# Kernel optimization log

Hardware: AMD Instinct MI355X
Metric: run time of the kernel (lower is better)

## Reference

```python
import jax, jax.numpy as jnp
import numpy as np

TOP_K = 4
EPS = 1e-12  # torch F.normalize eps

def _l2_normalize(x):
    n = jnp.linalg.norm(x, axis=-1, keepdims=True)
    return x / jnp.maximum(n, EPS)

def setup_inputs() -> dict:
    key = jax.random.key(0)
    k1, k2, k3 = jax.random.split(key, 3)
    queries = jax.random.normal(k1, (8192, 768), dtype=jnp.float32)
    # nn.init.uniform_(-1, 1) for both params
    keys = jax.random.uniform(k2, (64, 768), dtype=jnp.float32, minval=-1.0, maxval=1.0)
    prompts = jax.random.uniform(k3, (64, 8, 768), dtype=jnp.float32, minval=-1.0, maxval=1.0)
    return {"queries": queries, "keys": keys, "prompts": prompts}

def reference(queries, keys, prompts):
    N = queries.shape[0]
    pool_size, prompt_dim, embed_dim = prompts.shape
    qn = _l2_normalize(queries)              # [N, D]
    kn = _l2_normalize(keys)                 # [P, D]
    sim = qn @ kn.T                          # [N, P] cosine similarity
    _, idx = jax.lax.top_k(sim, TOP_K)       # [N, K] per-query top-k key ids
    # histogram vote over the pool (equivalent to torch.unique(..., return_counts) + pad)
    counts = jnp.zeros((pool_size,), jnp.int32).at[idx.reshape(-1)].add(1)
    _, top_idx = jax.lax.top_k(counts, TOP_K)  # [K] most-voted prompt ids
    # gather prompts, broadcast to every query: [N, K*prompt_dim, embed_dim]
    sel = prompts[top_idx].reshape(1, TOP_K * prompt_dim, embed_dim)
    selected_prompts = jnp.broadcast_to(sel, (N, TOP_K * prompt_dim, embed_dim))
    selected_keys = kn[top_idx]              # [K, D], same for all queries
    loss = jnp.sum(selected_keys[None, :, :] * qn[:, None, :]) / N
    return selected_prompts, loss
```

## Files before the change

kernel.cpp:

```cpp
#include <hip/hip_runtime.h>
#include <math.h>

#define NQ 8192
#define D 768
#define DF4 (D/4)
#define P 64
#define K 4
#define PD 8
#define QPB 16
#define NBLK (NQ/QPB)
#define ROWS_PER_WB 4
#define F4_PER_K ((PD*D)/4)
#define F4_PER_N ((K*PD*D)/4)
#define SEL_ELEMS ((size_t)NQ * K * PD * D)

typedef float f32x4 __attribute__((ext_vector_type(4)));

__global__ __launch_bounds__(256) void normalize_keys(const float* __restrict__ keys,
                                                      f32x4* __restrict__ knT4,
                                                      int* __restrict__ g_counts) {
    int b = blockIdx.x;
    int t = threadIdx.x;
    if (b == 0 && t < P) g_counts[t] = 0;
    __shared__ float red[256];
    float ss = 0.f;
    for (int j = t; j < D; j += 256) { float v = keys[b * D + j]; ss = fmaf(v, v, ss); }
    red[t] = ss; __syncthreads();
    for (int s = 128; s > 0; s >>= 1) { if (t < s) red[t] += red[t + s]; __syncthreads(); }
    float inv = 1.f / fmaxf(sqrtf(red[0]), 1e-12f);
    if (t < DF4) {
        f32x4 v;
        v.x = keys[b * D + 4 * t + 0] * inv;
        v.y = keys[b * D + 4 * t + 1] * inv;
        v.z = keys[b * D + 4 * t + 2] * inv;
        v.w = keys[b * D + 4 * t + 3] * inv;
        knT4[t * P + b] = v;
    }
}

__global__ __launch_bounds__(256) void sim_topk(const float* __restrict__ q,
                                                const f32x4* __restrict__ knT4,
                                                int* __restrict__ g_counts,
                                                float* __restrict__ colpartial) {
    __shared__ float4 qt[QPB * DF4];
    __shared__ float  simw[4][QPB][P];
    __shared__ float  colw[4][P];
    __shared__ int    cnt[P];
    int t = threadIdx.x;
    int w = t >> 6, lane = t & 63;
    int qbase = blockIdx.x * QPB;

    const float4* q4 = (const float4*)q + (size_t)qbase * DF4;
    #pragma unroll
    for (int i = 0; i < (QPB * DF4) / 256; ++i) qt[t + i * 256] = q4[t + i * 256];
    if (t < P) cnt[t] = 0;
    __syncthreads();

    float acc[QPB];
    #pragma unroll
    for (int i = 0; i < QPB; ++i) acc[i] = 0.f;
    int d4base = w * 48;
    const f32x4* kq = knT4 + (size_t)d4base * P;
    #pragma unroll 4
    for (int d4 = 0; d4 < 48; ++d4) {
        f32x4 kv = kq[d4 * P + lane];
        #pragma unroll
        for (int qi = 0; qi < QPB; ++qi) {
            float4 v = qt[qi * DF4 + d4base + d4];
            acc[qi] = fmaf(v.x, kv.x, fmaf(v.y, kv.y, fmaf(v.z, kv.z, fmaf(v.w, kv.w, acc[qi]))));
        }
    }
    #pragma unroll
    for (int qi = 0; qi < QPB; ++qi) simw[w][qi][lane] = acc[qi];
    __syncthreads();

    float colacc = 0.f;
    #pragma unroll
    for (int s = 0; s < 4; ++s) {
        int qi = w * 4 + s;
        float dot = simw[0][qi][lane] + simw[1][qi][lane] + simw[2][qi][lane] + simw[3][qi][lane];
        float ss = 0.f;
        #pragma unroll
        for (int j = 0; j < 3; ++j) {
            float4 v = qt[qi * DF4 + lane + j * 64];
            ss = fmaf(v.x, v.x, fmaf(v.y, v.y, fmaf(v.z, v.z, fmaf(v.w, v.w, ss))));
        }
        #pragma unroll
        for (int off = 32; off > 0; off >>= 1) ss += __shfl_xor(ss, off);
        float inv = 1.f / fmaxf(sqrtf(ss), 1e-12f);
        float sim = dot * inv;
        colacc += sim;
        float mv = sim;
        int w0, w1, w2, w3;
        #pragma unroll
        for (int r = 0; r < 4; ++r) {
            float v = mv; int idx = lane;
            #pragma unroll
            for (int off = 32; off > 0; off >>= 1) {
                float ov = __shfl_xor(v, off);
                int   oi = __shfl_xor(idx, off);
                if (ov > v || (ov == v && oi < idx)) { v = ov; idx = oi; }
            }
            if (r == 0) w0 = idx; else if (r == 1) w1 = idx; else if (r == 2) w2 = idx; else w3 = idx;
            if (lane == idx) mv = -INFINITY;
        }
        if (lane == 0) {
            atomicAdd(&cnt[w0], 1); atomicAdd(&cnt[w1], 1);
            atomicAdd(&cnt[w2], 1); atomicAdd(&cnt[w3], 1);
        }
    }
    colw[w][lane] = colacc;
    __syncthreads();

    if (t < P) {
        atomicAdd(&g_counts[t], cnt[t]);
        colpartial[(size_t)blockIdx.x * P + t] = colw[0][t] + colw[1][t] + colw[2][t] + colw[3][t];
    }
}

__global__ __launch_bounds__(256) void finalize(const float* __restrict__ colpartial,
                                                const int* __restrict__ g_counts,
                                                int* __restrict__ top_idx,
                                                float* __restrict__ loss_out) {
    __shared__ float colg[4][P];
    __shared__ float colsum[P];
    int t = threadIdx.x;
    int key = t & 63, grp = t >> 6;
    float s = 0.f;
    for (int b = grp * (NBLK / 4); b < (grp + 1) * (NBLK / 4); ++b)
        s += colpartial[(size_t)b * P + key];
    colg[grp][key] = s;
    __syncthreads();
    if (t < P) colsum[t] = colg[0][t] + colg[1][t] + colg[2][t] + colg[3][t];
    __syncthreads();
    if (t == 0) {
        int c[P];
        #pragma unroll
        for (int i = 0; i < P; ++i) c[i] = g_counts[i];
        float loss = 0.f;
        for (int r = 0; r < K; ++r) {
            int best = 0, bv = c[0];
            for (int i = 1; i < P; ++i) if (c[i] > bv) { bv = c[i]; best = i; }
            top_idx[r] = best; loss += colsum[best]; c[best] = -1;
        }
        loss_out[0] = loss / (float)NQ;
    }
}

__global__ __launch_bounds__(256) void writer(const float* __restrict__ prompts,
                                              const int* __restrict__ top_idx,
                                              float* __restrict__ out) {
    int b = blockIdx.x;
    int t = threadIdx.x;
    int i0 = top_idx[0], i1 = top_idx[1], i2 = top_idx[2], i3 = top_idx[3];
    const f32x4* p4 = (const f32x4*)prompts;
    f32x4* o4 = (f32x4*)out + (size_t)b * ROWS_PER_WB * F4_PER_N;
    #pragma unroll
    for (int k = 0; k < K; ++k) {
        int src = (k == 0) ? i0 : (k == 1) ? i1 : (k == 2) ? i2 : i3;
        const f32x4* sp = p4 + (size_t)src * F4_PER_K;
        f32x4 v0 = sp[0 * 256 + t], v1 = sp[1 * 256 + t], v2 = sp[2 * 256 + t];
        f32x4 v3 = sp[3 * 256 + t], v4 = sp[4 * 256 + t], v5 = sp[5 * 256 + t];
        #pragma unroll
        for (int r = 0; r < ROWS_PER_WB; ++r) {
            f32x4* dst = o4 + (size_t)r * F4_PER_N + k * F4_PER_K;
            dst[0 * 256 + t] = v0; dst[1 * 256 + t] = v1; dst[2 * 256 + t] = v2;
            dst[3 * 256 + t] = v3; dst[4 * 256 + t] = v4; dst[5 * 256 + t] = v5;
        }
    }
}

extern "C" void kernel_launch(void* const* d_in, const int* in_sizes, int n_in,
                              void* d_out, int out_size, void* d_ws, size_t ws_size,
                              hipStream_t stream) {
    const float* queries = (const float*)d_in[0];
    const float* keys    = (const float*)d_in[1];
    const float* prompts = (const float*)d_in[2];
    float* out = (float*)d_out;
    float* ws  = (float*)d_ws;

    f32x4* knT4       = (f32x4*)ws;
    float* colpartial = ws + 49152;
    int*   counts     = (int*)(ws + 49152 + 32768);
    int*   top_idx    = (int*)(ws + 49152 + 32768 + 64);

    normalize_keys<<<P, 256, 0, stream>>>(keys, knT4, counts);
    sim_topk<<<NBLK, 256, 0, stream>>>(queries, knT4, counts, colpartial);
    finalize<<<1, 256, 0, stream>>>(colpartial, counts, top_idx, out + SEL_ELEMS);
    writer<<<NQ / ROWS_PER_WB, 256, 0, stream>>>(prompts, top_idx, out);
}
```

Baseline: 214.6 us.

## Fuse finalize into sim kernel via last-block reduction and split dot work per wave

```diff
diff --git a/kernel.cpp b/kernel.cpp
--- a/kernel.cpp
+++ b/kernel.cpp
@@ -18,10 +18,14 @@
 
 __global__ __launch_bounds__(256) void normalize_keys(const float* __restrict__ keys,
                                                       f32x4* __restrict__ knT4,
-                                                      int* __restrict__ g_counts) {
+                                                      int* __restrict__ g_counts,
+                                                      int* __restrict__ done) {
     int b = blockIdx.x;
     int t = threadIdx.x;
-    if (b == 0 && t < P) g_counts[t] = 0;
+    if (b == 0) {
+        if (t < P) g_counts[t] = 0;
+        if (t == P) *done = 0;
+    }
     __shared__ float red[256];
     float ss = 0.f;
     for (int j = t; j < D; j += 256) { float v = keys[b * D + j]; ss = fmaf(v, v, ss); }
@@ -38,14 +42,20 @@
     }
 }
 
-__global__ __launch_bounds__(256) void sim_topk(const float* __restrict__ q,
-                                                const f32x4* __restrict__ knT4,
-                                                int* __restrict__ g_counts,
-                                                float* __restrict__ colpartial) {
+__global__ __launch_bounds__(256) void sim_sel(const float* __restrict__ q,
+                                               const f32x4* __restrict__ knT4,
+                                               int* __restrict__ g_counts,
+                                               float* __restrict__ colpartial,
+                                               int* __restrict__ done,
+                                               int* __restrict__ top_idx,
+                                               float* __restrict__ loss_out) {
     __shared__ float4 qt[QPB * DF4];
-    __shared__ float  simw[4][QPB][P];
     __shared__ float  colw[4][P];
     __shared__ int    cnt[P];
+    __shared__ int    lastblk;
+    __shared__ float  colg[4][P];
+    __shared__ float  colsum[P];
+    __shared__ int    cfin[P];
     int t = threadIdx.x;
     int w = t >> 6, lane = t & 63;
     int qbase = blockIdx.x * QPB;
@@ -56,29 +66,21 @@
     if (t < P) cnt[t] = 0;
     __syncthreads();
 
-    float acc[QPB];
-    #pragma unroll
-    for (int i = 0; i < QPB; ++i) acc[i] = 0.f;
-    int d4base = w * 48;
-    const f32x4* kq = knT4 + (size_t)d4base * P;
+    float acc[4] = {0.f, 0.f, 0.f, 0.f};
     #pragma unroll 4
-    for (int d4 = 0; d4 < 48; ++d4) {
-        f32x4 kv = kq[d4 * P + lane];
+    for (int d4 = 0; d4 < DF4; ++d4) {
+        f32x4 kv = knT4[d4 * P + lane];
         #pragma unroll
-        for (int qi = 0; qi < QPB; ++qi) {
-            float4 v = qt[qi * DF4 + d4base + d4];
-            acc[qi] = fmaf(v.x, kv.x, fmaf(v.y, kv.y, fmaf(v.z, kv.z, fmaf(v.w, kv.w, acc[qi]))));
+        for (int s = 0; s < 4; ++s) {
+            float4 v = qt[(w * 4 + s) * DF4 + d4];
+            acc[s] = fmaf(v.x, kv.x, fmaf(v.y, kv.y, fmaf(v.z, kv.z, fmaf(v.w, kv.w, acc[s]))));
         }
     }
-    #pragma unroll
-    for (int qi = 0; qi < QPB; ++qi) simw[w][qi][lane] = acc[qi];
-    __syncthreads();
 
     float colacc = 0.f;
     #pragma unroll
     for (int s = 0; s < 4; ++s) {
         int qi = w * 4 + s;
-        float dot = simw[0][qi][lane] + simw[1][qi][lane] + simw[2][qi][lane] + simw[3][qi][lane];
         float ss = 0.f;
         #pragma unroll
         for (int j = 0; j < 3; ++j) {
@@ -88,7 +90,7 @@
         #pragma unroll
         for (int off = 32; off > 0; off >>= 1) ss += __shfl_xor(ss, off);
         float inv = 1.f / fmaxf(sqrtf(ss), 1e-12f);
-        float sim = dot * inv;
+        float sim = acc[s] * inv;
         colacc += sim;
         float mv = sim;
         int w0, w1, w2, w3;
@@ -116,27 +118,26 @@
         atomicAdd(&g_counts[t], cnt[t]);
         colpartial[(size_t)blockIdx.x * P + t] = colw[0][t] + colw[1][t] + colw[2][t] + colw[3][t];
     }
-}
+    __threadfence();
+    __syncthreads();
+    if (t == 0) lastblk = (atomicAdd(done, 1) == NBLK - 1);
+    __syncthreads();
+    if (!lastblk) return;
 
-__global__ __launch_bounds__(256) void finalize(const float* __restrict__ colpartial,
-                                                const int* __restrict__ g_counts,
-                                                int* __restrict__ top_idx,
-                                                float* __restrict__ loss_out) {
-    __shared__ float colg[4][P];
-    __shared__ float colsum[P];
-    int t = threadIdx.x;
-    int key = t & 63, grp = t >> 6;
-    float s = 0.f;
-    for (int b = grp * (NBLK / 4); b < (grp + 1) * (NBLK / 4); ++b)
-        s += colpartial[(size_t)b * P + key];
-    colg[grp][key] = s;
+    __threadfence();
+    float ssum = 0.f;
+    #pragma unroll 8
+    for (int b = w * (NBLK / 4); b < (w + 1) * (NBLK / 4); ++b)
+        ssum += colpartial[(size_t)b * P + lane];
+    colg[w][lane] = ssum;
+    if (t < P) cfin[t] = atomicAdd(&g_counts[t], 0);
     __syncthreads();
     if (t < P) colsum[t] = colg[0][t] + colg[1][t] + colg[2][t] + colg[3][t];
     __syncthreads();
     if (t == 0) {
         int c[P];
         #pragma unroll
-        for (int i = 0; i < P; ++i) c[i] = g_counts[i];
+        for (int i = 0; i < P; ++i) c[i] = cfin[i];
         float loss = 0.f;
         for (int r = 0; r < K; ++r) {
             int best = 0, bv = c[0];
@@ -159,13 +160,13 @@
     for (int k = 0; k < K; ++k) {
         int src = (k == 0) ? i0 : (k == 1) ? i1 : (k == 2) ? i2 : i3;
         const f32x4* sp = p4 + (size_t)src * F4_PER_K;
-        f32x4 v0 = sp[0 * 256 + t], v1 = sp[1 * 256 + t], v2 = sp[2 * 256 + t];
-        f32x4 v3 = sp[3 * 256 + t], v4 = sp[4 * 256 + t], v5 = sp[5 * 256 + t];
         #pragma unroll
-        for (int r = 0; r < ROWS_PER_WB; ++r) {
-            f32x4* dst = o4 + (size_t)r * F4_PER_N + k * F4_PER_K;
-            dst[0 * 256 + t] = v0; dst[1 * 256 + t] = v1; dst[2 * 256 + t] = v2;
-            dst[3 * 256 + t] = v3; dst[4 * 256 + t] = v4; dst[5 * 256 + t] = v5;
+        for (int jj = 0; jj < 6; ++jj) {
+            int off = jj * 256 + t;
+            f32x4 v = sp[off];
+            #pragma unroll
+            for (int r = 0; r < ROWS_PER_WB; ++r)
+                o4[(size_t)r * F4_PER_N + k * F4_PER_K + off] = v;
         }
     }
 }
@@ -183,9 +184,10 @@
     float* colpartial = ws + 49152;
     int*   counts     = (int*)(ws + 49152 + 32768);
     int*   top_idx    = (int*)(ws + 49152 + 32768 + 64);
+    int*   done       = (int*)(ws + 49152 + 32768 + 64 + 4);
 
-    normalize_keys<<<P, 256, 0, stream>>>(keys, knT4, counts);
-    sim_topk<<<NBLK, 256, 0, stream>>>(queries, knT4, counts, colpartial);
-    finalize<<<1, 256, 0, stream>>>(colpartial, counts, top_idx, out + SEL_ELEMS);
+    normalize_keys<<<P, 256, 0, stream>>>(keys, knT4, counts, done);
+    sim_sel<<<NBLK, 256, 0, stream>>>(queries, knT4, counts, colpartial, done, top_idx,
+                                      out + SEL_ELEMS);
     writer<<<NQ / ROWS_PER_WB, 256, 0, stream>>>(prompts, top_idx, out);
 }
```

Result: slower. 227.6 us (+6.1%).

## Remap sim_topk thread tiling to query-by-key-group and enlarge writer rows

Applied to the files above, without the earlier changes.

```diff
diff --git a/kernel.cpp b/kernel.cpp
--- a/kernel.cpp
+++ b/kernel.cpp
@@ -4,12 +4,13 @@
 #define NQ 8192
 #define D 768
 #define DF4 (D/4)
+#define QSTRIDE 193
 #define P 64
 #define K 4
 #define PD 8
 #define QPB 16
 #define NBLK (NQ/QPB)
-#define ROWS_PER_WB 4
+#define ROWS_PER_WB 16
 #define F4_PER_K ((PD*D)/4)
 #define F4_PER_N ((K*PD*D)/4)
 #define SEL_ELEMS ((size_t)NQ * K * PD * D)
@@ -42,8 +43,8 @@
                                                 const f32x4* __restrict__ knT4,
                                                 int* __restrict__ g_counts,
                                                 float* __restrict__ colpartial) {
-    __shared__ float4 qt[QPB * DF4];
-    __shared__ float  simw[4][QPB][P];
+    __shared__ float4 qt[QPB * QSTRIDE];
+    __shared__ float4 simq4[QPB * 17];
     __shared__ float  colw[4][P];
     __shared__ int    cnt[P];
     int t = threadIdx.x;
@@ -52,37 +53,46 @@
 
     const float4* q4 = (const float4*)q + (size_t)qbase * DF4;
     #pragma unroll
-    for (int i = 0; i < (QPB * DF4) / 256; ++i) qt[t + i * 256] = q4[t + i * 256];
+    for (int i = 0; i < (QPB * DF4) / 256; ++i) {
+        int idx = t + i * 256;
+        int qi = idx / DF4, j = idx - qi * DF4;
+        qt[qi * QSTRIDE + j] = q4[idx];
+    }
     if (t < P) cnt[t] = 0;
     __syncthreads();
 
-    float acc[QPB];
-    #pragma unroll
-    for (int i = 0; i < QPB; ++i) acc[i] = 0.f;
-    int d4base = w * 48;
-    const f32x4* kq = knT4 + (size_t)d4base * P;
+    int qi = t & 15, kg = t >> 4;
+    const float4* qrow = qt + qi * QSTRIDE;
+    const f32x4* kbase = knT4 + 4 * kg;
+    float a0 = 0.f, a1 = 0.f, a2 = 0.f, a3 = 0.f;
     #pragma unroll 4
-    for (int d4 = 0; d4 < 48; ++d4) {
-        f32x4 kv = kq[d4 * P + lane];
-        #pragma unroll
-        for (int qi = 0; qi < QPB; ++qi) {
-            float4 v = qt[qi * DF4 + d4base + d4];
-            acc[qi] = fmaf(v.x, kv.x, fmaf(v.y, kv.y, fmaf(v.z, kv.z, fmaf(v.w, kv.w, acc[qi]))));
-        }
-    }
-    #pragma unroll
-    for (int qi = 0; qi < QPB; ++qi) simw[w][qi][lane] = acc[qi];
-    __syncthreads();
-
+    for (int d4 = 0; d4 < DF4; ++d4) {
+        float4 qv = qrow[d4];
+        f32x4 k0 = kbase[d4 * P + 0];
+        f32x4 k1 = kbase[d4 * P + 1];
+        f32x4 k2 = kbase[d4 * P + 2];
+        f32x4 k3 = kbase[d4 * P + 3];
+        a0 = fmaf(qv.x, k0.x, fmaf(qv.y, k0.y, fmaf(qv.z, k0.z, fmaf(qv.w, k0.w, a0))));
+        a1 = fmaf(qv.x, k1.x, fmaf(qv.y, k1.y, fmaf(qv.z, k1.z, fmaf(qv.w, k1.w, a1))));
+        a2 = fmaf(qv.x, k2.x, fmaf(qv.y, k2.y, fmaf(qv.z, k2.z, fmaf(qv.w, k2.w, a2))));
+        a3 = fmaf(qv.x, k3.x, fmaf(qv.y, k3.y, fmaf(qv.z, k3.z, fmaf(qv.w, k3.w, a3))));
+    }
+    {
+        float4 v; v.x = a0; v.y = a1; v.z = a2; v.w = a3;
+        simq4[qi * 17 + kg] = v;
+    }
+    __syncthreads();
+
+    const float* simq = (const float*)simq4;
     float colacc = 0.f;
     #pragma unroll
     for (int s = 0; s < 4; ++s) {
-        int qi = w * 4 + s;
-        float dot = simw[0][qi][lane] + simw[1][qi][lane] + simw[2][qi][lane] + simw[3][qi][lane];
+        int qe = w * 4 + s;
+        float dot = simq[qe * 68 + lane];
         float ss = 0.f;
         #pragma unroll
         for (int j = 0; j < 3; ++j) {
-            float4 v = qt[qi * DF4 + lane + j * 64];
+            float4 v = qt[qe * QSTRIDE + lane + j * 64];
             ss = fmaf(v.x, v.x, fmaf(v.y, v.y, fmaf(v.z, v.z, fmaf(v.w, v.w, ss))));
         }
         #pragma unroll
```

Result: slower. 233.2 us (+8.7%).
